# Kernel optimization log

Measured on AMD Instinct MI355X. Metric: run time of the kernel, lower is better.

Reference implementation:

```python
import jax, jax.numpy as jnp
import numpy as np

EMBED_DIM = 1024
NUM_HEADS = 16
HEAD_DIM = EMBED_DIM // NUM_HEADS


def setup_inputs() -> dict:
    key = jax.random.key(0)
    kx, kq, kk, kv, kbq, kbk, kbv = jax.random.split(key, 7)
    s = 1.0 / np.sqrt(EMBED_DIM)
    return {
        "x": jax.random.normal(kx, (4, 2048, EMBED_DIM), dtype=jnp.float32),
        "Wq": jax.random.uniform(kq, (EMBED_DIM, EMBED_DIM), jnp.float32, -s, s),
        "bq": jax.random.uniform(kbq, (EMBED_DIM,), jnp.float32, -s, s),
        "Wk": jax.random.uniform(kk, (EMBED_DIM, EMBED_DIM), jnp.float32, -s, s),
        "bk": jax.random.uniform(kbk, (EMBED_DIM,), jnp.float32, -s, s),
        "Wv": jax.random.uniform(kv, (EMBED_DIM, EMBED_DIM), jnp.float32, -s, s),
        "bv": jax.random.uniform(kbv, (EMBED_DIM,), jnp.float32, -s, s),
    }


def reference(x, Wq, bq, Wk, bk, Wv, bv):
    B, S, E = x.shape
    H, D = NUM_HEADS, HEAD_DIM
    # QKV projections; reshape to (B, H, S, D)
    def proj(W, b):
        return (x @ W + b).reshape(B, S, H, D).transpose(0, 2, 1, 3)
    Q = proj(Wq, bq)
    K = proj(Wk, bk)
    V = proj(Wv, bv)
    scale = jnp.asarray(np.sqrt(D), x.dtype)
    scores = jnp.einsum("bhqd,bhkd->bhqk", Q, K) / scale
    attn = jax.nn.softmax(scores, axis=-1)
    out = jnp.einsum("bhqk,bhkd->bhqd", attn, V)
    return out.transpose(0, 2, 1, 3).reshape(B, S, E)
```

## Files before the change

kernel.cpp:

```cpp
#include <hip/hip_runtime.h>
#include <math.h>

typedef unsigned short u16;
typedef __bf16 bf16x8 __attribute__((ext_vector_type(8)));
typedef float f32x4 __attribute__((ext_vector_type(4)));
typedef u16 u16x8 __attribute__((ext_vector_type(8)));
typedef u16 u16x4 __attribute__((ext_vector_type(4)));
typedef short s16x4 __attribute__((ext_vector_type(4)));
typedef unsigned u32x2 __attribute__((ext_vector_type(2)));
typedef unsigned u32x4 __attribute__((ext_vector_type(4)));

#define BB 4
#define SS 2048
#define EE 1024
#define HH 16
#define DH 64
#define PLANE (SS * DH)

__device__ __forceinline__ u16 f32_to_bf16(float f) {
  unsigned u = __builtin_bit_cast(unsigned, f);
  u += 0x7fffu + ((u >> 16) & 1u);
  return (u16)(u >> 16);
}

__device__ __forceinline__ unsigned pack_bf16_trunc(float lo, float hi) {
  return __builtin_amdgcn_perm(__builtin_bit_cast(unsigned, hi),
                               __builtin_bit_cast(unsigned, lo), 0x07060302u);
}

__device__ __forceinline__ void async_copy16(const void* g, void* lds) {
  __builtin_amdgcn_global_load_lds(
      (const __attribute__((address_space(1))) void*)g,
      (__attribute__((address_space(3))) void*)lds, 16, 0, 0);
}

__device__ __forceinline__ float ex2(float x) {
#if __has_builtin(__builtin_amdgcn_exp2f)
  return __builtin_amdgcn_exp2f(x);
#else
  return exp2f(x);
#endif
}

__global__ void cvt_x_kernel(const float* __restrict__ x, u16* __restrict__ xb) {
  int i = (blockIdx.x * 256 + threadIdx.x) * 8;
  float4 a = *(const float4*)(x + i);
  float4 c = *(const float4*)(x + i + 4);
  u16x8 o;
  o[0] = f32_to_bf16(a.x); o[1] = f32_to_bf16(a.y);
  o[2] = f32_to_bf16(a.z); o[3] = f32_to_bf16(a.w);
  o[4] = f32_to_bf16(c.x); o[5] = f32_to_bf16(c.y);
  o[6] = f32_to_bf16(c.z); o[7] = f32_to_bf16(c.w);
  *(u16x8*)(xb + i) = o;
}

__global__ void cvt_w_kernel(const float* __restrict__ Wq, const float* __restrict__ Wk,
                             const float* __restrict__ Wv, u16* __restrict__ wb) {
  __shared__ u16 T[64 * 72];
  int mat = blockIdx.z;
  const float* W = (mat == 0) ? Wq : ((mat == 1) ? Wk : Wv);
  int e0 = blockIdx.x * 64, k0 = blockIdx.y * 64;
  int t = threadIdx.x;
  int tr = t >> 4, tc = t & 15;
  for (int i = 0; i < 4; ++i) {
    int k = i * 16 + tr;
    float4 v = *(const float4*)(W + (k0 + k) * EE + e0 + tc * 4);
    T[(tc * 4 + 0) * 72 + k] = f32_to_bf16(v.x);
    T[(tc * 4 + 1) * 72 + k] = f32_to_bf16(v.y);
    T[(tc * 4 + 2) * 72 + k] = f32_to_bf16(v.z);
    T[(tc * 4 + 3) * 72 + k] = f32_to_bf16(v.w);
  }
  __syncthreads();
  u16* out = wb + (size_t)(mat * EE + e0) * EE + k0;
  for (int i = 0; i < 4; ++i) {
    int e = i * 16 + tr;
    u16x4 v = *(u16x4*)&T[e * 72 + tc * 4];
    *(u16x4*)(out + e * EE + tc * 4) = v;
  }
}

__global__ __launch_bounds__(256) void qkv_gemm_kernel(
    const u16* __restrict__ A, const u16* __restrict__ Bt,
    const float* __restrict__ bq, const float* __restrict__ bk,
    const float* __restrict__ bv, u16* __restrict__ qkv) {
  __shared__ u16 As0[128 * 32], Bs0[128 * 32];
  __shared__ u16 As1[128 * 32], Bs1[128 * 32];
  int tid = threadIdx.x;
  int lane = tid & 63, w = tid >> 6;
  int ln = lane & 15, quad = lane >> 4;
  int wm = w & 1, wn = w >> 1;
  int wg = blockIdx.y * 24 + blockIdx.x;
  int swz = (wg & 7) * 192 + (wg >> 3);
  int bn = swz % 24, bm = swz / 24;
  const u16* Ag = A + (size_t)bm * 128 * EE;
  const u16* Bg = Bt + (size_t)bn * 128 * EE;

  f32x4 acc[4][4] = {};

  auto STAGE = [&](u16* AsD, u16* BsD, int kt) {
    int k0 = kt * 32;
#pragma unroll
    for (int i = 0; i < 2; ++i) {
      int c = w * 128 + i * 64 + lane;
      int row = c >> 2, kc = (c & 3) * 8;
      async_copy16(Ag + row * EE + k0 + kc, AsD + (w * 128 + i * 64) * 8);
      async_copy16(Bg + row * EE + k0 + kc, BsD + (w * 128 + i * 64) * 8);
    }
  };

  auto TILE = [&](const u16* AsB, const u16* BsB) {
    __builtin_amdgcn_s_setprio(1);
    bf16x8 af[4], bfr[4];
#pragma unroll
    for (int mi = 0; mi < 4; ++mi)
      af[mi] = *(const bf16x8*)&AsB[(wm * 64 + mi * 16 + ln) * 32 + quad * 8];
#pragma unroll
    for (int ni = 0; ni < 4; ++ni)
      bfr[ni] = *(const bf16x8*)&BsB[(wn * 64 + ni * 16 + ln) * 32 + quad * 8];
#pragma unroll
    for (int mi = 0; mi < 4; ++mi)
#pragma unroll
      for (int ni = 0; ni < 4; ++ni)
        acc[mi][ni] = __builtin_amdgcn_mfma_f32_16x16x32_bf16(af[mi], bfr[ni],
                                                              acc[mi][ni], 0, 0, 0);
    __builtin_amdgcn_s_setprio(0);
  };

  STAGE(As0, Bs0, 0);
#pragma unroll 1
  for (int kt = 0; kt < 32; kt += 2) {
    STAGE(As1, Bs1, kt + 1);
    asm volatile("s_waitcnt vmcnt(4)" ::: "memory");
    __builtin_amdgcn_sched_barrier(0);
    __builtin_amdgcn_s_barrier();
    __builtin_amdgcn_sched_barrier(0);
    TILE(As0, Bs0);
    __builtin_amdgcn_s_barrier();
    if (kt + 2 < 32) {
      STAGE(As0, Bs0, kt + 2);
      asm volatile("s_waitcnt vmcnt(4)" ::: "memory");
    } else {
      asm volatile("s_waitcnt vmcnt(0)" ::: "memory");
    }
    __builtin_amdgcn_sched_barrier(0);
    __builtin_amdgcn_s_barrier();
    __builtin_amdgcn_sched_barrier(0);
    TILE(As1, Bs1);
    __builtin_amdgcn_s_barrier();
  }

  int mat = bn >> 3;
  const float* bias = (mat == 0) ? bq : ((mat == 1) ? bk : bv);
  int b = bm >> 4;
  if (mat < 2) {
    float scl = (mat == 0) ? 0.18033688011112042f : 1.0f;
    int base0 = (mat * BB + b) * HH * PLANE;
    for (int ni = 0; ni < 4; ++ni) {
      int e = (bn & 7) * 128 + wn * 64 + ni * 16 + ln;
      float bve = bias[e];
      int hh = e >> 6, d = e & 63;
      int cb = base0 + hh * PLANE + d;
      for (int mi = 0; mi < 4; ++mi) {
        int s0 = (bm & 15) * 128 + wm * 64 + mi * 16 + quad * 4;
        for (int r = 0; r < 4; ++r)
          qkv[cb + (s0 + r) * DH] = f32_to_bf16((acc[mi][ni][r] + bve) * scl);
      }
    }
  } else {
    size_t base0 = (size_t)(2 * BB + b) * HH * PLANE;
    for (int ni = 0; ni < 4; ++ni) {
      int e = (bn & 7) * 128 + wn * 64 + ni * 16 + ln;
      float bve = bias[e];
      int hh = e >> 6, d = e & 63;
      size_t cb = base0 + (size_t)hh * PLANE + (size_t)d * SS;
      for (int mi = 0; mi < 4; ++mi) {
        int s0 = (bm & 15) * 128 + wm * 64 + mi * 16 + quad * 4;
        u16x4 vv;
        for (int r = 0; r < 4; ++r) vv[r] = f32_to_bf16(acc[mi][ni][r] + bve);
        *(u16x4*)(qkv + cb + s0) = vv;
      }
    }
  }
}

__global__ __launch_bounds__(256, 4) void attn_kernel(const u16* __restrict__ qkv,
                                                      float* __restrict__ out) {
  __shared__ u16 Ks0[64 * 64], Ks1[64 * 64];
  __shared__ u16 Vs0[64 * 64], Vs1[64 * 64];
  int qb = blockIdx.x, h = blockIdx.y, b = blockIdx.z;
  int t = threadIdx.x;
  int lane = t & 63, w = t >> 6;
  int ln = lane & 15, quad = lane >> 4;
  int k7 = ln & 7;
  int q0 = quad & 1, q1 = quad >> 1;
  int bh = b * HH + h;
  const u16* Qg = qkv + (size_t)bh * PLANE + qb * 128 * DH;
  const u16* Kg = qkv + (size_t)(BB * HH + bh) * PLANE;
  const u16* Vg = qkv + (size_t)(2 * BB * HH + bh) * PLANE;

  int r8 = lane >> 3, c8 = lane & 7;
  int sc8 = (c8 ^ r8) * 8;

  auto STAGE = [&](u16* KsD, u16* VsD, int kt) {
    const u16* Kt = Kg + kt * 64 * DH;
    const u16* Vt = Vg + kt * 64;
#pragma unroll
    for (int i = 0; i < 2; ++i) {
      int row = w * 16 + i * 8 + r8;
      async_copy16(Kt + row * DH + sc8, KsD + (w * 16 + i * 8) * DH);
      async_copy16(Vt + row * SS + sc8, VsD + (w * 16 + i * 8) * DH);
    }
  };

  bf16x8 bq[2][2];
#pragma unroll
  for (int rb = 0; rb < 2; ++rb)
#pragma unroll
    for (int s = 0; s < 2; ++s)
      bq[rb][s] = *(const bf16x8*)(Qg + (w * 32 + rb * 16 + ln) * DH + s * 32 + quad * 8);

  u32x4 ow;
  ow[0] = ow[1] = ow[2] = ow[3] = 0x3F803F80u;
  bf16x8 ones8 = __builtin_bit_cast(bf16x8, ow);

  const f32x4 kz = {};
  f32x4 o[4][2] = {};
  f32x4 lacc[2] = {};

  int ks0 = (quad ^ k7) * 8;
  int ks1 = ks0 ^ 32;

  auto TILE = [&](const u16* Ksb, const u16* Vsb) {
    __builtin_amdgcn_s_setprio(1);
    f32x4 s[2][4];
#pragma unroll
    for (int g = 0; g < 4; ++g) {
      const u16* krow = Ksb + (g * 16 + ln) * DH;
      bf16x8 kf0 = *(const bf16x8*)(krow + ks0);
      bf16x8 kf1 = *(const bf16x8*)(krow + ks1);
      s[0][g] = __builtin_amdgcn_mfma_f32_16x16x32_bf16(kf0, bq[0][0], kz, 0, 0, 0);
      s[0][g] = __builtin_amdgcn_mfma_f32_16x16x32_bf16(kf1, bq[0][1], s[0][g], 0, 0, 0);
      s[1][g] = __builtin_amdgcn_mfma_f32_16x16x32_bf16(kf0, bq[1][0], kz, 0, 0, 0);
      s[1][g] = __builtin_amdgcn_mfma_f32_16x16x32_bf16(kf1, bq[1][1], s[1][g], 0, 0, 0);
    }
    bf16x8 af[2][2];
#pragma unroll
    for (int rb = 0; rb < 2; ++rb) {
      unsigned Wd[4][2];
#pragma unroll
      for (int g = 0; g < 4; ++g) {
        Wd[g][0] = pack_bf16_trunc(ex2(s[rb][g][0]), ex2(s[rb][g][1]));
        Wd[g][1] = pack_bf16_trunc(ex2(s[rb][g][2]), ex2(s[rb][g][3]));
      }
#pragma unroll
      for (int G = 0; G < 2; ++G) {
        u32x4 aw;
        aw[0] = Wd[2 * G][0];     aw[1] = Wd[2 * G][1];
        aw[2] = Wd[2 * G + 1][0]; aw[3] = Wd[2 * G + 1][1];
        af[rb][G] = __builtin_bit_cast(bf16x8, aw);
      }
      lacc[rb] = __builtin_amdgcn_mfma_f32_16x16x32_bf16(af[rb][0], ones8, lacc[rb], 0, 0, 0);
      lacc[rb] = __builtin_amdgcn_mfma_f32_16x16x32_bf16(af[rb][1], ones8, lacc[rb], 0, 0, 0);
    }
#pragma unroll
    for (int G = 0; G < 2; ++G) {
      int uLo = ((4 * G + q1) ^ k7) * 8 + 4 * q0;
      int uHi = ((4 * G + q1 + 2) ^ k7) * 8 + 4 * q0;
#pragma unroll
      for (int dg = 0; dg < 4; ++dg) {
        const u16* vrow = Vsb + (dg * 16 + ln) * DH;
        u32x2 lo = *(const u32x2*)(vrow + uLo);
        u32x2 hi = *(const u32x2*)(vrow + uHi);
        u32x4 vv;
        vv[0] = lo[0]; vv[1] = lo[1]; vv[2] = hi[0]; vv[3] = hi[1];
        bf16x8 vf = __builtin_bit_cast(bf16x8, vv);
        o[dg][0] = __builtin_amdgcn_mfma_f32_16x16x32_bf16(af[0][G], vf, o[dg][0], 0, 0, 0);
        o[dg][1] = __builtin_amdgcn_mfma_f32_16x16x32_bf16(af[1][G], vf, o[dg][1], 0, 0, 0);
      }
    }
    __builtin_amdgcn_s_setprio(0);
  };

  STAGE(Ks0, Vs0, 0);
#pragma unroll 1
  for (int kt = 0; kt < 32; kt += 2) {
    STAGE(Ks1, Vs1, kt + 1);
    asm volatile("s_waitcnt vmcnt(4)" ::: "memory");
    __builtin_amdgcn_sched_barrier(0);
    __builtin_amdgcn_s_barrier();
    __builtin_amdgcn_sched_barrier(0);
    TILE(Ks0, Vs0);
    __builtin_amdgcn_s_barrier();
    if (kt + 2 < 32) {
      STAGE(Ks0, Vs0, kt + 2);
      asm volatile("s_waitcnt vmcnt(4)" ::: "memory");
    } else {
      asm volatile("s_waitcnt vmcnt(0)" ::: "memory");
    }
    __builtin_amdgcn_sched_barrier(0);
    __builtin_amdgcn_s_barrier();
    __builtin_amdgcn_sched_barrier(0);
    TILE(Ks1, Vs1);
    __builtin_amdgcn_s_barrier();
  }

  int sb = qb * 128 + w * 32;
  float* og = out + (size_t)b * SS * EE + (size_t)h * DH;
#pragma unroll
  for (int rb = 0; rb < 2; ++rb)
#pragma unroll
    for (int r = 0; r < 4; ++r) {
      float ir = 1.0f / lacc[rb][r];
      size_t qrow = (size_t)(sb + rb * 16 + quad * 4 + r);
#pragma unroll
      for (int dg = 0; dg < 4; ++dg)
        og[qrow * EE + dg * 16 + ln] = o[dg][rb][r] * ir;
    }
}

extern "C" void kernel_launch(void* const* d_in, const int* in_sizes, int n_in,
                              void* d_out, int out_size, void* d_ws, size_t ws_size,
                              hipStream_t stream) {
  (void)in_sizes; (void)n_in; (void)out_size; (void)ws_size;
  const float* x  = (const float*)d_in[0];
  const float* Wq = (const float*)d_in[1];
  const float* bq = (const float*)d_in[2];
  const float* Wk = (const float*)d_in[3];
  const float* bk = (const float*)d_in[4];
  const float* Wv = (const float*)d_in[5];
  const float* bv = (const float*)d_in[6];
  float* out = (float*)d_out;

  u16* xb  = (u16*)d_out;
  u16* wb  = xb + (size_t)BB * SS * EE;
  u16* qkv = (u16*)d_ws;

  cvt_x_kernel<<<dim3((BB * SS * EE) / (256 * 8)), 256, 0, stream>>>(x, xb);
  cvt_w_kernel<<<dim3(16, 16, 3), 256, 0, stream>>>(Wq, Wk, Wv, wb);
  qkv_gemm_kernel<<<dim3(24, 64), 256, 0, stream>>>(xb, wb, bq, bk, bv, qkv);
  attn_kernel<<<dim3(SS / 128, HH, BB), 256, 0, stream>>>(qkv, out);
}
```

Measured before the change: 247.2 us.

## Triple-buffer QKV GEMM LDS tiles with one barrier per k-step

Moves the QKV projection GEMM from double-buffered to triple-buffered LDS staging. Each k-step now waits on the oldest copy, issues one barrier, prefetches two tiles ahead and then computes, replacing the two barriers per tile. It also drops the workgroup-index swizzle in favour of plain blockIdx mapping. The goal is fewer barrier stalls and deeper load/compute overlap, at the cost of 8KB more shared memory per block (possible occupancy loss) and possibly worse L2 locality without the swizzle.

```diff
diff --git a/kernel.cpp b/kernel.cpp
--- a/kernel.cpp
+++ b/kernel.cpp
@@ -85,13 +85,12 @@
     const float* __restrict__ bv, u16* __restrict__ qkv) {
   __shared__ u16 As0[128 * 32], Bs0[128 * 32];
   __shared__ u16 As1[128 * 32], Bs1[128 * 32];
+  __shared__ u16 As2[128 * 32], Bs2[128 * 32];
   int tid = threadIdx.x;
   int lane = tid & 63, w = tid >> 6;
   int ln = lane & 15, quad = lane >> 4;
   int wm = w & 1, wn = w >> 1;
-  int wg = blockIdx.y * 24 + blockIdx.x;
-  int swz = (wg & 7) * 192 + (wg >> 3);
-  int bn = swz % 24, bm = swz / 24;
+  int bn = blockIdx.x, bm = blockIdx.y;
   const u16* Ag = A + (size_t)bm * 128 * EE;
   const u16* Bg = Bt + (size_t)bn * 128 * EE;
 
@@ -126,28 +125,29 @@
     __builtin_amdgcn_s_setprio(0);
   };
 
+#define GSTEP(VM, AsC, BsC, AsN, BsN, ktn)                     \
+  do {                                                         \
+    asm volatile("s_waitcnt vmcnt(" #VM ")" ::: "memory");     \
+    __builtin_amdgcn_sched_barrier(0);                         \
+    __builtin_amdgcn_s_barrier();                              \
+    __builtin_amdgcn_sched_barrier(0);                         \
+    if ((ktn) < 32) STAGE(AsN, BsN, ktn);                      \
+    __builtin_amdgcn_sched_barrier(0);                         \
+    TILE(AsC, BsC);                                            \
+  } while (0)
+
   STAGE(As0, Bs0, 0);
+  STAGE(As1, Bs1, 1);
 #pragma unroll 1
-  for (int kt = 0; kt < 32; kt += 2) {
-    STAGE(As1, Bs1, kt + 1);
-    asm volatile("s_waitcnt vmcnt(4)" ::: "memory");
-    __builtin_amdgcn_sched_barrier(0);
-    __builtin_amdgcn_s_barrier();
-    __builtin_amdgcn_sched_barrier(0);
-    TILE(As0, Bs0);
-    __builtin_amdgcn_s_barrier();
-    if (kt + 2 < 32) {
-      STAGE(As0, Bs0, kt + 2);
-      asm volatile("s_waitcnt vmcnt(4)" ::: "memory");
-    } else {
-      asm volatile("s_waitcnt vmcnt(0)" ::: "memory");
-    }
-    __builtin_amdgcn_sched_barrier(0);
-    __builtin_amdgcn_s_barrier();
-    __builtin_amdgcn_sched_barrier(0);
-    TILE(As1, Bs1);
-    __builtin_amdgcn_s_barrier();
-  }
+  for (int t = 0; t < 10; ++t) {
+    int kt = t * 3;
+    GSTEP(4, As0, Bs0, As2, Bs2, kt + 2);
+    GSTEP(4, As1, Bs1, As0, Bs0, kt + 3);
+    GSTEP(4, As2, Bs2, As1, Bs1, kt + 4);
+  }
+  GSTEP(4, As0, Bs0, As2, Bs2, 32);
+  GSTEP(0, As1, Bs1, As2, Bs2, 32);
+#undef GSTEP
 
   int mat = bn >> 3;
   const float* bias = (mat == 0) ? bq : ((mat == 1) ? bk : bv);
```

Measured after the change: 245.9 us. Within noise of the previous version (-0.5%).

## Deepen QKV GEMM K-tile to 64 with swizzled LDS and remap attention blocks

Applied to the files above, without the earlier changes.

The QKV GEMM K-tile doubles from 32 to 64, with an XOR-swizzled LDS layout for the async copies and fragment reads. This halves the barrier and wait count per K and should reduce LDS bank conflicts. The GEMM drops its block-order swizzle and uses plain grid indices, while the attention kernel now maps blocks so each XCD handles contiguous (batch, head) planes for K/V cache locality. LDS use doubles, which could lower occupancy, and the exp2 fallback becomes inline asm, which likely has no effect because the builtin path is taken.

```diff
diff --git a/kernel.cpp b/kernel.cpp
--- a/kernel.cpp
+++ b/kernel.cpp
@@ -38,7 +38,9 @@
 #if __has_builtin(__builtin_amdgcn_exp2f)
   return __builtin_amdgcn_exp2f(x);
 #else
-  return exp2f(x);
+  float r;
+  asm("v_exp_f32 %0, %1\n\ts_nop 1" : "=v"(r) : "v"(x));
+  return r;
 #endif
 }
 
@@ -83,62 +85,73 @@
     const u16* __restrict__ A, const u16* __restrict__ Bt,
     const float* __restrict__ bq, const float* __restrict__ bk,
     const float* __restrict__ bv, u16* __restrict__ qkv) {
-  __shared__ u16 As0[128 * 32], Bs0[128 * 32];
-  __shared__ u16 As1[128 * 32], Bs1[128 * 32];
+  __shared__ u16 As0[128 * 64], Bs0[128 * 64];
+  __shared__ u16 As1[128 * 64], Bs1[128 * 64];
   int tid = threadIdx.x;
   int lane = tid & 63, w = tid >> 6;
   int ln = lane & 15, quad = lane >> 4;
   int wm = w & 1, wn = w >> 1;
-  int wg = blockIdx.y * 24 + blockIdx.x;
-  int swz = (wg & 7) * 192 + (wg >> 3);
-  int bn = swz % 24, bm = swz / 24;
+  int bn = blockIdx.x, bm = blockIdx.y;
   const u16* Ag = A + (size_t)bm * 128 * EE;
   const u16* Bg = Bt + (size_t)bn * 128 * EE;
 
+  int r8 = lane >> 3, c8 = lane & 7;
+  int sc8 = (c8 ^ r8) * 8;
+
   f32x4 acc[4][4] = {};
 
   auto STAGE = [&](u16* AsD, u16* BsD, int kt) {
-    int k0 = kt * 32;
-#pragma unroll
-    for (int i = 0; i < 2; ++i) {
-      int c = w * 128 + i * 64 + lane;
-      int row = c >> 2, kc = (c & 3) * 8;
-      async_copy16(Ag + row * EE + k0 + kc, AsD + (w * 128 + i * 64) * 8);
-      async_copy16(Bg + row * EE + k0 + kc, BsD + (w * 128 + i * 64) * 8);
+    int k0 = kt * 64;
+#pragma unroll
+    for (int i = 0; i < 4; ++i) {
+      int row0 = i * 32 + w * 8;
+      async_copy16(Ag + (row0 + r8) * EE + k0 + sc8, AsD + (i * 256 + w * 64) * 8);
+      async_copy16(Bg + (row0 + r8) * EE + k0 + sc8, BsD + (i * 256 + w * 64) * 8);
     }
   };
+
+  int k7 = ln & 7;
+  int ks0 = (quad ^ k7) * 8;
+  int ks1 = ks0 ^ 32;
 
   auto TILE = [&](const u16* AsB, const u16* BsB) {
     __builtin_amdgcn_s_setprio(1);
-    bf16x8 af[4], bfr[4];
-#pragma unroll
-    for (int mi = 0; mi < 4; ++mi)
-      af[mi] = *(const bf16x8*)&AsB[(wm * 64 + mi * 16 + ln) * 32 + quad * 8];
-#pragma unroll
-    for (int ni = 0; ni < 4; ++ni)
-      bfr[ni] = *(const bf16x8*)&BsB[(wn * 64 + ni * 16 + ln) * 32 + quad * 8];
-#pragma unroll
-    for (int mi = 0; mi < 4; ++mi)
-#pragma unroll
-      for (int ni = 0; ni < 4; ++ni)
-        acc[mi][ni] = __builtin_amdgcn_mfma_f32_16x16x32_bf16(af[mi], bfr[ni],
+    bf16x8 b0[4], b1[4];
+#pragma unroll
+    for (int ni = 0; ni < 4; ++ni) {
+      const u16* br = BsB + (wn * 64 + ni * 16 + ln) * 64;
+      b0[ni] = *(const bf16x8*)(br + ks0);
+      b1[ni] = *(const bf16x8*)(br + ks1);
+    }
+#pragma unroll
+    for (int mi = 0; mi < 4; ++mi) {
+      const u16* ar = AsB + (wm * 64 + mi * 16 + ln) * 64;
+      bf16x8 a0 = *(const bf16x8*)(ar + ks0);
+      bf16x8 a1 = *(const bf16x8*)(ar + ks1);
+#pragma unroll
+      for (int ni = 0; ni < 4; ++ni) {
+        acc[mi][ni] = __builtin_amdgcn_mfma_f32_16x16x32_bf16(a0, b0[ni],
                                                               acc[mi][ni], 0, 0, 0);
+        acc[mi][ni] = __builtin_amdgcn_mfma_f32_16x16x32_bf16(a1, b1[ni],
+                                                              acc[mi][ni], 0, 0, 0);
+      }
+    }
     __builtin_amdgcn_s_setprio(0);
   };
 
   STAGE(As0, Bs0, 0);
 #pragma unroll 1
-  for (int kt = 0; kt < 32; kt += 2) {
+  for (int kt = 0; kt < 16; kt += 2) {
     STAGE(As1, Bs1, kt + 1);
-    asm volatile("s_waitcnt vmcnt(4)" ::: "memory");
+    asm volatile("s_waitcnt vmcnt(8)" ::: "memory");
     __builtin_amdgcn_sched_barrier(0);
     __builtin_amdgcn_s_barrier();
     __builtin_amdgcn_sched_barrier(0);
     TILE(As0, Bs0);
     __builtin_amdgcn_s_barrier();
-    if (kt + 2 < 32) {
+    if (kt + 2 < 16) {
       STAGE(As0, Bs0, kt + 2);
-      asm volatile("s_waitcnt vmcnt(4)" ::: "memory");
+      asm volatile("s_waitcnt vmcnt(8)" ::: "memory");
     } else {
       asm volatile("s_waitcnt vmcnt(0)" ::: "memory");
     }
@@ -187,13 +200,16 @@
                                                       float* __restrict__ out) {
   __shared__ u16 Ks0[64 * 64], Ks1[64 * 64];
   __shared__ u16 Vs0[64 * 64], Vs1[64 * 64];
-  int qb = blockIdx.x, h = blockIdx.y, b = blockIdx.z;
+  int wg = blockIdx.x + (blockIdx.y << 4) + (blockIdx.z << 8);
+  int xcd = wg & 7, idx = wg >> 3;
+  int bh = xcd * 8 + (idx >> 4);
+  int qb = idx & 15;
+  int h = bh & 15, b = bh >> 4;
   int t = threadIdx.x;
   int lane = t & 63, w = t >> 6;
   int ln = lane & 15, quad = lane >> 4;
   int k7 = ln & 7;
   int q0 = quad & 1, q1 = quad >> 1;
-  int bh = b * HH + h;
   const u16* Qg = qkv + (size_t)bh * PLANE + qb * 128 * DH;
   const u16* Kg = qkv + (size_t)(BB * HH + bh) * PLANE;
   const u16* Vg = qkv + (size_t)(2 * BB * HH + bh) * PLANE;
```

Measured after the change: 244.7 us. Within noise of the previous version (-1.0%).
